# Kernel optimization log

Measured on AMD Instinct MI355X. Metric: run time of the kernel, lower is better.

The kernel has to match this reference:

```python
import jax, jax.numpy as jnp
import numpy as np

N, M = 50000, 800000
INP_DIM, HID_DIM = 256, 96
K, FAC = 8, 12          # init_k capsules, fac_dim = HID_DIM // K
ROUTIT, TAU = 6, 1.0
NUM_LAYERS = 4
EPS = 1e-12


def l2norm(x):
    # L2-normalize along the last (per-capsule feature) axis
    return x / jnp.sqrt(jnp.sum(x * x, axis=-1, keepdims=True) + EPS)


def setup_inputs() -> dict:
    key = jax.random.key(0)
    k1, k2, k3 = jax.random.split(key, 3)
    X = jax.random.normal(k1, (N, INP_DIM), dtype=jnp.float32)
    edges = jax.random.randint(k2, (2, M), 0, N)  # [2, m]: (src, dst)
    # InitDisenLayer: K per-capsule linear projections inp_dim -> fac_dim
    W_init = jax.random.normal(k3, (K, INP_DIM, FAC), dtype=jnp.float32) * (1.0 / np.sqrt(INP_DIM))
    b_init = jnp.zeros((K, FAC), dtype=jnp.float32)
    return {"X": X, "edges": edges, "W_init": W_init, "b_init": b_init}


def _routing_layer(z_flat, src, dst):
    # Neighborhood routing (Ma et al. 2019): z_flat [n, K*FAC]
    n = z_flat.shape[0]
    z = l2norm(z_flat.reshape(n, K, FAC))  # normalized per-capsule features
    c = z                                  # cluster centers init
    for _ in range(ROUTIT):
        # attention logit per edge per capsule: z_src . c_dst / tau
        att = jnp.einsum('ekd,ekd->ek', z[src], c[dst]) / TAU   # [m, K]
        p = jax.nn.softmax(att, axis=1)                          # over capsules
        agg = jax.ops.segment_sum(p[:, :, None] * z[src], dst, num_segments=n)  # [n,K,FAC]
        c = l2norm(z + agg)
    return c.reshape(n, K * FAC)


def reference(X, edges, W_init, b_init):
    # InitDisenLayer: per-capsule linear -> relu -> L2 normalize
    Z = jax.nn.relu(jnp.einsum('ni,kio->nko', X, W_init) + b_init)  # [n, K, FAC]
    Z = l2norm(Z).reshape(X.shape[0], -1)                           # [n, K*FAC]
    src, dst = edges[0], edges[1]
    for _ in range(NUM_LAYERS):
        Z = _routing_layer(Z, src, dst)
        Z = jax.nn.relu(Z)  # dropout is identity in eval mode
    return Z  # [n, K*FAC]; note: classifier is unused in the original forward
```

## Files before the change

kernel.cpp:

```cpp
#include <hip/hip_runtime.h>
#include <math.h>

#define N_NODES 50000
#define M_EDGES 800000
#define INP 256
#define KCAP 8
#define FAC 12
#define KF 96
#define ROUTIT 6
#define DMAX 24

#define OFF_ZA      0u
#define OFF_ZB      19200000u
#define OFF_ROWPTR  38400000u
#define OFF_PARTIAL 38600016u
#define OFF_CURSOR  38800016u
#define OFF_BSUMS   39000016u
#define OFF_CSR     39001040u
#define OFF_WT      42201040u

__global__ void wt_transpose(const float* __restrict__ W, float* __restrict__ Wt) {
    int idx = blockIdx.x * 256 + threadIdx.x;
    if (idx >= INP * KF) return;
    int i = idx / KF, kf = idx % KF;
    int k = kf / FAC, f = kf % FAC;
    Wt[i * KF + kf] = W[(k * INP + i) * FAC + f];
}

__global__ __launch_bounds__(192) void init_proj(const float* __restrict__ X,
                                                 const float* __restrict__ Wt,
                                                 const float* __restrict__ b,
                                                 float* __restrict__ Z0) {
    int nq  = threadIdx.x / 24;
    int kfq = threadIdx.x % 24;
    int nb  = blockIdx.x * 32 + nq * 4;
    int kf0 = kfq * 4;

    int nn[4];
    #pragma unroll
    for (int m = 0; m < 4; ++m) {
        int n = nb + m;
        nn[m] = n < N_NODES ? n : N_NODES - 1;
    }

    float acc[4][4];
    #pragma unroll
    for (int m = 0; m < 4; ++m)
        #pragma unroll
        for (int cc = 0; cc < 4; ++cc) acc[m][cc] = 0.f;

    for (int i4 = 0; i4 < INP / 4; ++i4) {
        float4 xv[4];
        #pragma unroll
        for (int m = 0; m < 4; ++m)
            xv[m] = ((const float4*)(X + (size_t)nn[m] * INP))[i4];
        float4 wv[4];
        #pragma unroll
        for (int r = 0; r < 4; ++r)
            wv[r] = *(const float4*)(Wt + (size_t)(i4 * 4 + r) * KF + kf0);
        #pragma unroll
        for (int m = 0; m < 4; ++m) {
            acc[m][0] = fmaf(xv[m].x, wv[0].x, acc[m][0]);
            acc[m][1] = fmaf(xv[m].x, wv[0].y, acc[m][1]);
            acc[m][2] = fmaf(xv[m].x, wv[0].z, acc[m][2]);
            acc[m][3] = fmaf(xv[m].x, wv[0].w, acc[m][3]);
            acc[m][0] = fmaf(xv[m].y, wv[1].x, acc[m][0]);
            acc[m][1] = fmaf(xv[m].y, wv[1].y, acc[m][1]);
            acc[m][2] = fmaf(xv[m].y, wv[1].z, acc[m][2]);
            acc[m][3] = fmaf(xv[m].y, wv[1].w, acc[m][3]);
            acc[m][0] = fmaf(xv[m].z, wv[2].x, acc[m][0]);
            acc[m][1] = fmaf(xv[m].z, wv[2].y, acc[m][1]);
            acc[m][2] = fmaf(xv[m].z, wv[2].z, acc[m][2]);
            acc[m][3] = fmaf(xv[m].z, wv[2].w, acc[m][3]);
            acc[m][0] = fmaf(xv[m].w, wv[3].x, acc[m][0]);
            acc[m][1] = fmaf(xv[m].w, wv[3].y, acc[m][1]);
            acc[m][2] = fmaf(xv[m].w, wv[3].z, acc[m][2]);
            acc[m][3] = fmaf(xv[m].w, wv[3].w, acc[m][3]);
        }
    }

    float4 bv = *(const float4*)(b + kf0);
    #pragma unroll
    for (int m = 0; m < 4; ++m) {
        int n = nb + m;
        if (n < N_NODES) {
            float4 o;
            o.x = fmaxf(acc[m][0] + bv.x, 0.f);
            o.y = fmaxf(acc[m][1] + bv.y, 0.f);
            o.z = fmaxf(acc[m][2] + bv.z, 0.f);
            o.w = fmaxf(acc[m][3] + bv.w, 0.f);
            *(float4*)(Z0 + (size_t)n * KF + kf0) = o;
        }
    }
}

__global__ void prep_norm(const float* __restrict__ Z0, float* __restrict__ zb) {
    int cap = blockIdx.x * blockDim.x + threadIdx.x;
    if (cap >= N_NODES * KCAP) return;
    const float4* p = (const float4*)(Z0 + (size_t)cap * FAC);
    float4 a = p[0], bq = p[1], cq = p[2];
    float ss = a.x*a.x + a.y*a.y + a.z*a.z + a.w*a.w
             + bq.x*bq.x + bq.y*bq.y + bq.z*bq.z + bq.w*bq.w
             + cq.x*cq.x + cq.y*cq.y + cq.z*cq.z + cq.w*cq.w;
    float inv = rsqrtf(ss + 1e-12f);
    float4* o = (float4*)(zb + (size_t)cap * FAC);
    float4 r0, r1, r2;
    r0.x=a.x*inv;  r0.y=a.y*inv;  r0.z=a.z*inv;  r0.w=a.w*inv;
    r1.x=bq.x*inv; r1.y=bq.y*inv; r1.z=bq.z*inv; r1.w=bq.w*inv;
    r2.x=cq.x*inv; r2.y=cq.y*inv; r2.z=cq.z*inv; r2.w=cq.w*inv;
    o[0]=r0; o[1]=r1; o[2]=r2;
}

__global__ void hist(const int* __restrict__ dst, int* __restrict__ counts) {
    int e = blockIdx.x * 256 + threadIdx.x;
    if (e < M_EDGES) atomicAdd(&counts[dst[e]], 1);
}
__global__ void scan1(const int* __restrict__ counts, int* __restrict__ partial,
                      int* __restrict__ bsums) {
    __shared__ int s[256];
    int t = threadIdx.x;
    int i = blockIdx.x * 256 + t;
    int v = (i < N_NODES) ? counts[i] : 0;
    s[t] = v; __syncthreads();
    for (int off = 1; off < 256; off <<= 1) {
        int tmp = (t >= off) ? s[t - off] : 0;
        __syncthreads();
        s[t] += tmp;
        __syncthreads();
    }
    if (i < N_NODES) partial[i] = s[t];
    if (t == 255) bsums[blockIdx.x] = s[t];
}
__global__ void scan2(int* __restrict__ bs, int nb) {
    __shared__ int s[256];
    int t = threadIdx.x;
    int v = (t < nb) ? bs[t] : 0;
    s[t] = v; __syncthreads();
    for (int off = 1; off < 256; off <<= 1) {
        int tmp = (t >= off) ? s[t - off] : 0;
        __syncthreads();
        s[t] += tmp;
        __syncthreads();
    }
    if (t < nb) bs[t] = s[t] - v;
}
__global__ void finalize_rp(const int* __restrict__ partial, const int* __restrict__ boffs,
                            const int* __restrict__ counts,
                            int* __restrict__ row_ptr, int* __restrict__ cursor) {
    int i = blockIdx.x * 256 + threadIdx.x;
    if (i < N_NODES) {
        int incl = partial[i] + boffs[i >> 8];
        row_ptr[i + 1] = incl;
        cursor[i] = incl - counts[i];
    }
    if (i == 0) row_ptr[0] = 0;
}
__global__ void csr_fill(const int* __restrict__ src, const int* __restrict__ dst,
                         int* __restrict__ cursor, int* __restrict__ csr) {
    int e = blockIdx.x * 256 + threadIdx.x;
    if (e < M_EDGES) {
        int d = dst[e];
        int pos = atomicAdd(&cursor[d], 1);
        csr[pos] = src[e];
    }
}

__global__ __launch_bounds__(256, 3) void route(const float* __restrict__ zin,
                                                float* __restrict__ znext,
                                                float* __restrict__ dout,
                                                const int* __restrict__ row_ptr,
                                                const int* __restrict__ csr,
                                                int write_out) {
    int wid  = (blockIdx.x * 256 + threadIdx.x) >> 6;
    int lane = threadIdx.x & 63;
    int h  = lane >> 5;
    int gp = (lane >> 3) & 3;
    int k  = lane & 7;
    int node = wid * 2 + h;

    float z[12], c[12];
    {
        const float4* zr = (const float4*)(zin + (size_t)node * KF + k * FAC);
        #pragma unroll
        for (int q = 0; q < 3; ++q) {
            float4 t = zr[q];
            z[q*4+0]=t.x; z[q*4+1]=t.y; z[q*4+2]=t.z; z[q*4+3]=t.w;
        }
    }
    #pragma unroll
    for (int d = 0; d < 12; ++d) c[d] = z[d];

    int base = row_ptr[node];
    int deg  = row_ptr[node + 1] - base;
    int degc = deg < DMAX ? deg : DMAX;
    int dm = deg;
    dm = max(dm, __shfl_xor(dm, 32));
    bool hasTail = dm > DMAX;

    float zc[6][12];
    #pragma unroll
    for (int j = 0; j < 6; ++j) {
        int idx = j * 4 + gp;
        if (idx < degc) {
            int s = csr[base + idx];
            const float4* zs4 = (const float4*)(zin + (size_t)s * KF + k * FAC);
            #pragma unroll
            for (int q = 0; q < 3; ++q) {
                float4 t = zs4[q];
                zc[j][q*4+0]=t.x; zc[j][q*4+1]=t.y; zc[j][q*4+2]=t.z; zc[j][q*4+3]=t.w;
            }
        } else {
            #pragma unroll
            for (int d = 0; d < 12; ++d) zc[j][d] = 0.f;
        }
    }

    for (int it = 0; it < ROUTIT; ++it) {
        float agg[12];
        #pragma unroll
        for (int d = 0; d < 12; ++d) agg[d] = 0.f;

        #pragma unroll
        for (int half = 0; half < 2; ++half) {
            int j0 = half * 3;
            float ex[3], sm[3];
            #pragma unroll
            for (int jj = 0; jj < 3; ++jj) {
                float att = 0.f;
                #pragma unroll
                for (int d = 0; d < 12; ++d) att = fmaf(zc[j0+jj][d], c[d], att);
                ex[jj] = __expf(att);
                sm[jj] = ex[jj];
            }
            #pragma unroll
            for (int m = 1; m <= 4; m <<= 1) {
                #pragma unroll
                for (int jj = 0; jj < 3; ++jj) sm[jj] += __shfl_xor(sm[jj], m);
            }
            #pragma unroll
            for (int jj = 0; jj < 3; ++jj) {
                float p = __fdividef(ex[jj], sm[jj]);
                #pragma unroll
                for (int d = 0; d < 12; ++d) agg[d] = fmaf(p, zc[j0+jj][d], agg[d]);
            }
        }

        if (hasTail) {
            for (int t0 = DMAX; t0 < dm; t0 += 4) {
                int idx = t0 + gp;
                bool act = idx < deg;
                float zs[12];
                #pragma unroll
                for (int d = 0; d < 12; ++d) zs[d] = 0.f;
                if (act) {
                    int s = csr[base + idx];
                    const float4* zs4 = (const float4*)(zin + (size_t)s * KF + k * FAC);
                    #pragma unroll
                    for (int q = 0; q < 3; ++q) {
                        float4 t = zs4[q];
                        zs[q*4+0]=t.x; zs[q*4+1]=t.y; zs[q*4+2]=t.z; zs[q*4+3]=t.w;
                    }
                }
                float att = 0.f;
                #pragma unroll
                for (int d = 0; d < 12; ++d) att = fmaf(zs[d], c[d], att);
                float exv = __expf(att);
                float smv = exv;
                smv += __shfl_xor(smv, 1);
                smv += __shfl_xor(smv, 2);
                smv += __shfl_xor(smv, 4);
                float p = __fdividef(exv, smv);
                #pragma unroll
                for (int d = 0; d < 12; ++d) agg[d] = fmaf(p, zs[d], agg[d]);
            }
        }

        #pragma unroll
        for (int d = 0; d < 12; ++d) agg[d] += __shfl_xor(agg[d], 8);
        #pragma unroll
        for (int d = 0; d < 12; ++d) agg[d] += __shfl_xor(agg[d], 16);

        float ss = 0.f;
        float v[12];
        #pragma unroll
        for (int d = 0; d < 12; ++d) { v[d] = z[d] + agg[d]; ss = fmaf(v[d], v[d], ss); }
        float inv = rsqrtf(ss + 1e-12f);
        #pragma unroll
        for (int d = 0; d < 12; ++d) c[d] = v[d] * inv;
    }

    if (gp == 0) {
        float r[12], ss = 0.f;
        #pragma unroll
        for (int d = 0; d < 12; ++d) { r[d] = fmaxf(c[d], 0.f); ss = fmaf(r[d], r[d], ss); }
        if (write_out) {
            float* oo = dout + (size_t)node * KF + k * FAC;
            #pragma unroll
            for (int q = 0; q < 3; ++q) {
                float4 t;
                t.x = r[q*4+0]; t.y = r[q*4+1]; t.z = r[q*4+2]; t.w = r[q*4+3];
                ((float4*)oo)[q] = t;
            }
        } else {
            float inv = rsqrtf(ss + 1e-12f);
            float* zo = znext + (size_t)node * KF + k * FAC;
            #pragma unroll
            for (int q = 0; q < 3; ++q) {
                float4 t;
                t.x = r[q*4+0]*inv; t.y = r[q*4+1]*inv; t.z = r[q*4+2]*inv; t.w = r[q*4+3]*inv;
                ((float4*)zo)[q] = t;
            }
        }
    }
}

extern "C" void kernel_launch(void* const* d_in, const int* in_sizes, int n_in,
                              void* d_out, int out_size, void* d_ws, size_t ws_size,
                              hipStream_t stream) {
    const float* X     = (const float*)d_in[0];
    const int*   edges = (const int*)d_in[1];
    const float* W     = (const float*)d_in[2];
    const float* b     = (const float*)d_in[3];
    float* out = (float*)d_out;
    char* ws = (char*)d_ws;

    float* zA      = (float*)(ws + OFF_ZA);
    float* zB      = (float*)(ws + OFF_ZB);
    int*   row_ptr = (int*)(ws + OFF_ROWPTR);
    int*   partial = (int*)(ws + OFF_PARTIAL);
    int*   cursor  = (int*)(ws + OFF_CURSOR);
    int*   bsums   = (int*)(ws + OFF_BSUMS);
    int*   csr     = (int*)(ws + OFF_CSR);
    float* Wt      = (float*)(ws + OFF_WT);

    const int* src = edges;
    const int* dst = edges + M_EDGES;

    wt_transpose<<<96, 256, 0, stream>>>(W, Wt);
    init_proj<<<(N_NODES + 31) / 32, 192, 0, stream>>>(X, Wt, b, zB);
    prep_norm<<<(N_NODES * KCAP + 255) / 256, 256, 0, stream>>>(zB, zA);

    hipMemsetAsync(cursor, 0, N_NODES * sizeof(int), stream);
    hist<<<(M_EDGES + 255) / 256, 256, 0, stream>>>(dst, cursor);
    scan1<<<196, 256, 0, stream>>>(cursor, partial, bsums);
    scan2<<<1, 256, 0, stream>>>(bsums, 196);
    finalize_rp<<<196, 256, 0, stream>>>(partial, bsums, cursor, row_ptr, cursor);
    csr_fill<<<(M_EDGES + 255) / 256, 256, 0, stream>>>(src, dst, cursor, csr);

    route<<<6250, 256, 0, stream>>>(zA, zB, nullptr, row_ptr, csr, 0);
    route<<<6250, 256, 0, stream>>>(zB, zA, nullptr, row_ptr, csr, 0);
    route<<<6250, 256, 0, stream>>>(zA, zB, nullptr, row_ptr, csr, 0);
    route<<<6250, 256, 0, stream>>>(zB, zA, out, row_ptr, csr, 1);
}
```

Before: 673.0 us.

## Fuse init normalization into projection and cache routing neighbors in packed fp16

The init projection kernel is restructured so each thread computes 24 outputs for 4 nodes, and the per-capsule L2 normalization is fused in, which removes the separate prep_norm pass and its intermediate buffer round trip. In the routing kernel, cached neighbor capsule vectors are stored as packed fp16 pairs and the attention dot product uses fdot2, halving register use for the cache. Occupancy is raised to 4 blocks per SM. This trades precision in the attention logits and aggregation for lower register pressure and higher occupancy.

```diff
diff --git a/kernel.cpp b/kernel.cpp
--- a/kernel.cpp
+++ b/kernel.cpp
@@ -10,6 +10,14 @@
 #define ROUTIT 6
 #define DMAX 24
 
+typedef __fp16 h2 __attribute__((ext_vector_type(2)));
+
+#if __has_builtin(__builtin_amdgcn_fdot2)
+#define FDOT2(a, b, c) __builtin_amdgcn_fdot2((a), (b), (c), false)
+#else
+#define FDOT2(a, b, c) (fmaf((float)(a)[1], (float)(b)[1], fmaf((float)(a)[0], (float)(b)[0], (c))))
+#endif
+
 #define OFF_ZA      0u
 #define OFF_ZB      19200000u
 #define OFF_ROWPTR  38400000u
@@ -27,88 +35,97 @@
     Wt[i * KF + kf] = W[(k * INP + i) * FAC + f];
 }
 
-__global__ __launch_bounds__(192) void init_proj(const float* __restrict__ X,
-                                                 const float* __restrict__ Wt,
-                                                 const float* __restrict__ b,
-                                                 float* __restrict__ Z0) {
-    int nq  = threadIdx.x / 24;
-    int kfq = threadIdx.x % 24;
-    int nb  = blockIdx.x * 32 + nq * 4;
-    int kf0 = kfq * 4;
-
-    int nn[4];
-    #pragma unroll
-    for (int m = 0; m < 4; ++m) {
-        int n = nb + m;
-        nn[m] = n < N_NODES ? n : N_NODES - 1;
-    }
-
-    float acc[4][4];
+__global__ __launch_bounds__(256, 2) void init_proj(const float* __restrict__ X,
+                                                    const float* __restrict__ Wt,
+                                                    const float* __restrict__ b,
+                                                    float* __restrict__ zA) {
+    int gid    = blockIdx.x * 256 + threadIdx.x;
+    int quad   = gid >> 2;
+    int pairId = gid & 3;
+    if (quad >= N_NODES / 4) return;
+    int nb  = quad * 4;
+    int kf0 = pairId * 24;
+
+    float acc[4][24];
     #pragma unroll
     for (int m = 0; m < 4; ++m)
         #pragma unroll
-        for (int cc = 0; cc < 4; ++cc) acc[m][cc] = 0.f;
+        for (int q = 0; q < 24; ++q) acc[m][q] = 0.f;
+
+    const float4* X4 = (const float4*)X;
 
     for (int i4 = 0; i4 < INP / 4; ++i4) {
         float4 xv[4];
         #pragma unroll
         for (int m = 0; m < 4; ++m)
-            xv[m] = ((const float4*)(X + (size_t)nn[m] * INP))[i4];
-        float4 wv[4];
-        #pragma unroll
-        for (int r = 0; r < 4; ++r)
-            wv[r] = *(const float4*)(Wt + (size_t)(i4 * 4 + r) * KF + kf0);
-        #pragma unroll
-        for (int m = 0; m < 4; ++m) {
-            acc[m][0] = fmaf(xv[m].x, wv[0].x, acc[m][0]);
-            acc[m][1] = fmaf(xv[m].x, wv[0].y, acc[m][1]);
-            acc[m][2] = fmaf(xv[m].x, wv[0].z, acc[m][2]);
-            acc[m][3] = fmaf(xv[m].x, wv[0].w, acc[m][3]);
-            acc[m][0] = fmaf(xv[m].y, wv[1].x, acc[m][0]);
-            acc[m][1] = fmaf(xv[m].y, wv[1].y, acc[m][1]);
-            acc[m][2] = fmaf(xv[m].y, wv[1].z, acc[m][2]);
-            acc[m][3] = fmaf(xv[m].y, wv[1].w, acc[m][3]);
-            acc[m][0] = fmaf(xv[m].z, wv[2].x, acc[m][0]);
-            acc[m][1] = fmaf(xv[m].z, wv[2].y, acc[m][1]);
-            acc[m][2] = fmaf(xv[m].z, wv[2].z, acc[m][2]);
-            acc[m][3] = fmaf(xv[m].z, wv[2].w, acc[m][3]);
-            acc[m][0] = fmaf(xv[m].w, wv[3].x, acc[m][0]);
-            acc[m][1] = fmaf(xv[m].w, wv[3].y, acc[m][1]);
-            acc[m][2] = fmaf(xv[m].w, wv[3].z, acc[m][2]);
-            acc[m][3] = fmaf(xv[m].w, wv[3].w, acc[m][3]);
-        }
-    }
-
-    float4 bv = *(const float4*)(b + kf0);
+            xv[m] = X4[(size_t)(nb + m) * (INP / 4) + i4];
+
+        #pragma unroll
+        for (int r = 0; r < 4; ++r) {
+            const float4* wr = (const float4*)(Wt + (size_t)(i4 * 4 + r) * KF + kf0);
+            float4 w0 = wr[0], w1 = wr[1], w2 = wr[2], w3 = wr[3], w4 = wr[4], w5 = wr[5];
+            #pragma unroll
+            for (int m = 0; m < 4; ++m) {
+                float xs = (r == 0) ? xv[m].x : (r == 1) ? xv[m].y : (r == 2) ? xv[m].z : xv[m].w;
+                acc[m][0]  = fmaf(xs, w0.x, acc[m][0]);
+                acc[m][1]  = fmaf(xs, w0.y, acc[m][1]);
+                acc[m][2]  = fmaf(xs, w0.z, acc[m][2]);
+                acc[m][3]  = fmaf(xs, w0.w, acc[m][3]);
+                acc[m][4]  = fmaf(xs, w1.x, acc[m][4]);
+                acc[m][5]  = fmaf(xs, w1.y, acc[m][5]);
+                acc[m][6]  = fmaf(xs, w1.z, acc[m][6]);
+                acc[m][7]  = fmaf(xs, w1.w, acc[m][7]);
+                acc[m][8]  = fmaf(xs, w2.x, acc[m][8]);
+                acc[m][9]  = fmaf(xs, w2.y, acc[m][9]);
+                acc[m][10] = fmaf(xs, w2.z, acc[m][10]);
+                acc[m][11] = fmaf(xs, w2.w, acc[m][11]);
+                acc[m][12] = fmaf(xs, w3.x, acc[m][12]);
+                acc[m][13] = fmaf(xs, w3.y, acc[m][13]);
+                acc[m][14] = fmaf(xs, w3.z, acc[m][14]);
+                acc[m][15] = fmaf(xs, w3.w, acc[m][15]);
+                acc[m][16] = fmaf(xs, w4.x, acc[m][16]);
+                acc[m][17] = fmaf(xs, w4.y, acc[m][17]);
+                acc[m][18] = fmaf(xs, w4.z, acc[m][18]);
+                acc[m][19] = fmaf(xs, w4.w, acc[m][19]);
+                acc[m][20] = fmaf(xs, w5.x, acc[m][20]);
+                acc[m][21] = fmaf(xs, w5.y, acc[m][21]);
+                acc[m][22] = fmaf(xs, w5.z, acc[m][22]);
+                acc[m][23] = fmaf(xs, w5.w, acc[m][23]);
+            }
+        }
+    }
+
+    const float* bp = b + kf0;
+    float bb[24];
+    #pragma unroll
+    for (int q = 0; q < 24; ++q) bb[q] = bp[q];
+
     #pragma unroll
     for (int m = 0; m < 4; ++m) {
-        int n = nb + m;
-        if (n < N_NODES) {
-            float4 o;
-            o.x = fmaxf(acc[m][0] + bv.x, 0.f);
-            o.y = fmaxf(acc[m][1] + bv.y, 0.f);
-            o.z = fmaxf(acc[m][2] + bv.z, 0.f);
-            o.w = fmaxf(acc[m][3] + bv.w, 0.f);
-            *(float4*)(Z0 + (size_t)n * KF + kf0) = o;
-        }
-    }
-}
-
-__global__ void prep_norm(const float* __restrict__ Z0, float* __restrict__ zb) {
-    int cap = blockIdx.x * blockDim.x + threadIdx.x;
-    if (cap >= N_NODES * KCAP) return;
-    const float4* p = (const float4*)(Z0 + (size_t)cap * FAC);
-    float4 a = p[0], bq = p[1], cq = p[2];
-    float ss = a.x*a.x + a.y*a.y + a.z*a.z + a.w*a.w
-             + bq.x*bq.x + bq.y*bq.y + bq.z*bq.z + bq.w*bq.w
-             + cq.x*cq.x + cq.y*cq.y + cq.z*cq.z + cq.w*cq.w;
-    float inv = rsqrtf(ss + 1e-12f);
-    float4* o = (float4*)(zb + (size_t)cap * FAC);
-    float4 r0, r1, r2;
-    r0.x=a.x*inv;  r0.y=a.y*inv;  r0.z=a.z*inv;  r0.w=a.w*inv;
-    r1.x=bq.x*inv; r1.y=bq.y*inv; r1.z=bq.z*inv; r1.w=bq.w*inv;
-    r2.x=cq.x*inv; r2.y=cq.y*inv; r2.z=cq.z*inv; r2.w=cq.w*inv;
-    o[0]=r0; o[1]=r1; o[2]=r2;
+        float v[24];
+        float ssA = 0.f, ssB = 0.f;
+        #pragma unroll
+        for (int q = 0; q < 12; ++q) {
+            v[q] = fmaxf(acc[m][q] + bb[q], 0.f);
+            ssA = fmaf(v[q], v[q], ssA);
+        }
+        #pragma unroll
+        for (int q = 12; q < 24; ++q) {
+            v[q] = fmaxf(acc[m][q] + bb[q], 0.f);
+            ssB = fmaf(v[q], v[q], ssB);
+        }
+        float invA = rsqrtf(ssA + 1e-12f);
+        float invB = rsqrtf(ssB + 1e-12f);
+        float* zo = zA + (size_t)(nb + m) * KF + kf0;
+        #pragma unroll
+        for (int q4 = 0; q4 < 6; ++q4) {
+            float sc = (q4 < 3) ? invA : invB;
+            float4 t;
+            t.x = v[q4*4+0] * sc; t.y = v[q4*4+1] * sc;
+            t.z = v[q4*4+2] * sc; t.w = v[q4*4+3] * sc;
+            ((float4*)zo)[q4] = t;
+        }
+    }
 }
 
 __global__ void hist(const int* __restrict__ dst, int* __restrict__ counts) {
@@ -165,7 +182,7 @@
     }
 }
 
-__global__ __launch_bounds__(256, 3) void route(const float* __restrict__ zin,
+__global__ __launch_bounds__(256, 4) void route(const float* __restrict__ zin,
                                                 float* __restrict__ znext,
                                                 float* __restrict__ dout,
                                                 const int* __restrict__ row_ptr,
@@ -197,25 +214,32 @@
     dm = max(dm, __shfl_xor(dm, 32));
     bool hasTail = dm > DMAX;
 
-    float zc[6][12];
+    h2 zc[6][6];
     #pragma unroll
     for (int j = 0; j < 6; ++j) {
         int idx = j * 4 + gp;
         if (idx < degc) {
             int s = csr[base + idx];
             const float4* zs4 = (const float4*)(zin + (size_t)s * KF + k * FAC);
-            #pragma unroll
-            for (int q = 0; q < 3; ++q) {
-                float4 t = zs4[q];
-                zc[j][q*4+0]=t.x; zc[j][q*4+1]=t.y; zc[j][q*4+2]=t.z; zc[j][q*4+3]=t.w;
-            }
+            float4 t0 = zs4[0], t1 = zs4[1], t2 = zs4[2];
+            zc[j][0] = __builtin_amdgcn_cvt_pkrtz(t0.x, t0.y);
+            zc[j][1] = __builtin_amdgcn_cvt_pkrtz(t0.z, t0.w);
+            zc[j][2] = __builtin_amdgcn_cvt_pkrtz(t1.x, t1.y);
+            zc[j][3] = __builtin_amdgcn_cvt_pkrtz(t1.z, t1.w);
+            zc[j][4] = __builtin_amdgcn_cvt_pkrtz(t2.x, t2.y);
+            zc[j][5] = __builtin_amdgcn_cvt_pkrtz(t2.z, t2.w);
         } else {
             #pragma unroll
-            for (int d = 0; d < 12; ++d) zc[j][d] = 0.f;
+            for (int p = 0; p < 6; ++p) zc[j][p] = (h2)(__fp16)0.f;
         }
     }
 
     for (int it = 0; it < ROUTIT; ++it) {
+        h2 cp[6];
+        #pragma unroll
+        for (int p = 0; p < 6; ++p)
+            cp[p] = __builtin_amdgcn_cvt_pkrtz(c[2*p], c[2*p+1]);
+
         float agg[12];
         #pragma unroll
         for (int d = 0; d < 12; ++d) agg[d] = 0.f;
@@ -228,7 +252,7 @@
             for (int jj = 0; jj < 3; ++jj) {
                 float att = 0.f;
                 #pragma unroll
-                for (int d = 0; d < 12; ++d) att = fmaf(zc[j0+jj][d], c[d], att);
+                for (int p = 0; p < 6; ++p) att = FDOT2(zc[j0+jj][p], cp[p], att);
                 ex[jj] = __expf(att);
                 sm[jj] = ex[jj];
             }
@@ -239,9 +263,12 @@
             }
             #pragma unroll
             for (int jj = 0; jj < 3; ++jj) {
-                float p = __fdividef(ex[jj], sm[jj]);
-                #pragma unroll
-                for (int d = 0; d < 12; ++d) agg[d] = fmaf(p, zc[j0+jj][d], agg[d]);
+                float pw = __fdividef(ex[jj], sm[jj]);
+                #pragma unroll
+                for (int p = 0; p < 6; ++p) {
+                    agg[2*p+0] = fmaf(pw, (float)zc[j0+jj][p][0], agg[2*p+0]);
+                    agg[2*p+1] = fmaf(pw, (float)zc[j0+jj][p][1], agg[2*p+1]);
+                }
             }
         }
 
@@ -269,9 +296,9 @@
                 smv += __shfl_xor(smv, 1);
                 smv += __shfl_xor(smv, 2);
                 smv += __shfl_xor(smv, 4);
-                float p = __fdividef(exv, smv);
-                #pragma unroll
-                for (int d = 0; d < 12; ++d) agg[d] = fmaf(p, zs[d], agg[d]);
+                float pw = __fdividef(exv, smv);
+                #pragma unroll
+                for (int d = 0; d < 12; ++d) agg[d] = fmaf(pw, zs[d], agg[d]);
             }
         }
 
@@ -337,10 +364,9 @@
     const int* dst = edges + M_EDGES;
 
     wt_transpose<<<96, 256, 0, stream>>>(W, Wt);
-    init_proj<<<(N_NODES + 31) / 32, 192, 0, stream>>>(X, Wt, b, zB);
-    prep_norm<<<(N_NODES * KCAP + 255) / 256, 256, 0, stream>>>(zB, zA);
-
-    hipMemsetAsync(cursor, 0, N_NODES * sizeof(int), stream);
+    init_proj<<<(N_NODES / 4 * 4 + 255) / 256, 256, 0, stream>>>(X, Wt, b, zA);
+
+    (void)hipMemsetAsync(cursor, 0, N_NODES * sizeof(int), stream);
     hist<<<(M_EDGES + 255) / 256, 256, 0, stream>>>(dst, cursor);
     scan1<<<196, 256, 0, stream>>>(cursor, partial, bsums);
     scan2<<<1, 256, 0, stream>>>(bsums, 196);
```

Result: slower. 2.540 ms (+277.5%).
